# Optimization experiments

Measured on AMD Instinct MI355X. Metric: run time of the kernel, lower is better.

Reference implementation:

```python
import jax, jax.numpy as jnp
import numpy as np

N = 50000
E = 800000
D = 256
C = 8
H = 64
LN_EPS = 1e-5


def setup_inputs() -> dict:
    key = jax.random.key(0)
    ks = jax.random.split(key, 8)
    x = jax.random.normal(ks[0], (N, D), dtype=jnp.float32)
    edge_index = jax.random.randint(ks[1], (2, E), 0, N, dtype=jnp.int64)
    omega = jax.random.uniform(ks[2], (E, C), dtype=jnp.float32)
    # xavier-uniform-ish parameter init
    def xavier(k, shape, fan_in, fan_out):
        a = float(np.sqrt(6.0 / (fan_in + fan_out)))
        return jax.random.uniform(k, shape, dtype=jnp.float32, minval=-a, maxval=a)
    proj = xavier(ks[3], (D, C, H), D, C * H)          # layer-0 projection
    W1 = xavier(ks[4], (C, H, H), H, H)                # layer-0 channel weights
    W2 = xavier(ks[5], (C, H, H), H, H)                # layer-1 channel weights
    ln_gamma = jnp.ones((H,), dtype=jnp.float32)
    ln_beta = jnp.zeros((H,), dtype=jnp.float32)
    return {"x": x, "edge_index": edge_index, "omega": omega,
            "proj": proj, "W1": W1, "W2": W2,
            "ln_gamma": ln_gamma, "ln_beta": ln_beta}


def _conv(h, src, dst, omega, W):
    # h: [N, C, H]; per-channel weighted scatter-add then channel-specific bmm.
    outs = []
    for c in range(C):  # small fixed channel loop, mirrors original structure
        msg = omega[:, c, None] * h[src, c, :]                  # [E, H]
        outs.append(jax.ops.segment_sum(msg, dst, num_segments=N))
    h_next = jnp.stack(outs, axis=1)                            # [N, C, H]
    return jnp.einsum('nch,cho->nco', h_next, W)                # channel bmm


def _layernorm(h, gamma, beta):
    mu = jnp.mean(h, axis=-1, keepdims=True)
    var = jnp.mean(jnp.square(h - mu), axis=-1, keepdims=True)
    return (h - mu) * jax.lax.rsqrt(var + LN_EPS) * gamma + beta


def reference(x, edge_index, omega, proj, W1, W2, ln_gamma, ln_beta):
    src, dst = edge_index[0], edge_index[1]
    # layer 0: project raw features into channel space [N, C, H]
    h = (x @ proj.reshape(D, C * H)).reshape(N, C, H)
    h = _conv(h, src, dst, omega, W1)
    h = _layernorm(h, ln_gamma, ln_beta)
    h = jax.nn.relu(h)
    # layer 1 (last layer: no ReLU)
    h = _conv(h, src, dst, omega, W2)
    h = _layernorm(h, ln_gamma, ln_beta)
    return h
```

## Files before the change

### kernel.cpp

```cpp
#include <hip/hip_runtime.h>

#define NN 50000
#define NE 800000
#define DD 256
#define CC 8
#define HH 64
#define CHW 512
#define LN_EPS 1e-5f

typedef __attribute__((ext_vector_type(8))) __bf16 bf16x8;
typedef __attribute__((ext_vector_type(4))) float f32x4;

__device__ inline ushort f2bf(float f) {
  uint u = __float_as_uint(f);
  return (ushort)((u + 0x7fffu + ((u >> 16) & 1u)) >> 16);
}

__global__ __launch_bounds__(256) void fold_w1_kernel(
    const float* __restrict__ proj, const float* __restrict__ W1,
    ushort* __restrict__ projW1T) {
  __shared__ float wl[64];
  const int n = blockIdx.x;
  const int c = n >> 6, i = n & 63;
  const int tid = threadIdx.x;
  if (tid < 64) wl[tid] = W1[c * 4096 + tid * 64 + i];
  __syncthreads();
  const float* pr = proj + (size_t)tid * 512 + c * 64;
  float acc = 0.f;
#pragma unroll
  for (int k = 0; k < 64; ++k) acc += pr[k] * wl[k];
  projW1T[(size_t)n * 256 + tid] = f2bf(acc);
}

__global__ __launch_bounds__(256) void w2t_kernel(const float* __restrict__ W2,
                                                  ushort* __restrict__ W2T) {
  int c = blockIdx.x;
  for (int idx = threadIdx.x; idx < 4096; idx += 256) {
    int nn = idx >> 6, k = idx & 63;
    W2T[(size_t)c * 4096 + idx] = f2bf(W2[(size_t)c * 4096 + k * 64 + nn]);
  }
}

__global__ __launch_bounds__(256) void gemm_proj_kernel(
    const float* __restrict__ x, const ushort* __restrict__ BT,
    ushort* __restrict__ gout) {
  __shared__ ushort As[128 * 40];
  __shared__ ushort Bs[128 * 40];
  const int tid = threadIdx.x;
  const int lane = tid & 63, wv = tid >> 6;
  const int wm = wv >> 1, wn = wv & 1;
  const int lr = lane & 15, kg = lane >> 4;
  const int row0 = blockIdx.x * 128;
  const int col0 = blockIdx.y * 128;

  f32x4 acc[4][4];
#pragma unroll
  for (int i = 0; i < 4; ++i)
#pragma unroll
    for (int j = 0; j < 4; ++j) acc[i][j] = (f32x4){0.f, 0.f, 0.f, 0.f};

  for (int kk = 0; kk < 8; ++kk) {
    __syncthreads();
#pragma unroll
    for (int i = 0; i < 4; ++i) {
      int idx = tid + i * 256;
      int row = idx >> 3, quad = idx & 7;
      int rg = row0 + row;
      rg = rg < NN ? rg : NN - 1;
      float4 v = *(const float4*)(x + (size_t)rg * 256 + kk * 32 + quad * 4);
      ushort4 o = {f2bf(v.x), f2bf(v.y), f2bf(v.z), f2bf(v.w)};
      *(ushort4*)(As + row * 40 + quad * 4) = o;
    }
#pragma unroll
    for (int i = 0; i < 2; ++i) {
      int idx = tid + i * 256;
      int n = idx >> 2, quad = idx & 3;
      uint4 v = *(const uint4*)(BT + (size_t)(col0 + n) * 256 + kk * 32 + quad * 8);
      *(uint4*)(Bs + n * 40 + quad * 8) = v;
    }
    __syncthreads();
    bf16x8 a[4], b[4];
#pragma unroll
    for (int i = 0; i < 4; ++i)
      a[i] = *(const bf16x8*)(As + (wm * 64 + i * 16 + lr) * 40 + kg * 8);
#pragma unroll
    for (int j = 0; j < 4; ++j)
      b[j] = *(const bf16x8*)(Bs + (wn * 64 + j * 16 + lr) * 40 + kg * 8);
#pragma unroll
    for (int i = 0; i < 4; ++i)
#pragma unroll
      for (int j = 0; j < 4; ++j)
        acc[i][j] = __builtin_amdgcn_mfma_f32_16x16x32_bf16(a[i], b[j], acc[i][j], 0, 0, 0);
  }

  const int orow = kg * 4;
  const int ocol = lane & 15;
#pragma unroll
  for (int i = 0; i < 4; ++i) {
    int rg0 = row0 + wm * 64 + i * 16 + orow;
#pragma unroll
    for (int q = 0; q < 4; ++q) {
      int rg = rg0 + q;
      if (rg < NN) {
#pragma unroll
        for (int j = 0; j < 4; ++j) {
          gout[(size_t)rg * 512 + col0 + wn * 64 + j * 16 + ocol] = f2bf(acc[i][j][q]);
        }
      }
    }
  }
}

__global__ __launch_bounds__(256) void bmm_g_kernel(
    const ushort* __restrict__ h, const ushort* __restrict__ WT,
    ushort* __restrict__ g) {
  __shared__ ushort As[128 * 72];
  __shared__ ushort Bs[64 * 72];
  __shared__ float Cs[4][32 * 68];
  const int tid = threadIdx.x, lane = tid & 63, wv = tid >> 6;
  const int lr = lane & 15, kg = lane >> 4;
  const int n0 = blockIdx.x * 128;
  const int c = blockIdx.y;

#pragma unroll
  for (int i = 0; i < 4; ++i) {
    int idx = tid + i * 256;
    int row = idx >> 3, q = idx & 7;
    int rg = n0 + row;
    rg = rg < NN ? rg : NN - 1;
    *(uint4*)(As + row * 72 + q * 8) =
        *(const uint4*)(h + (size_t)rg * 512 + c * 64 + q * 8);
  }
#pragma unroll
  for (int i = 0; i < 2; ++i) {
    int idx = tid + i * 256;
    int row = idx >> 3, q = idx & 7;
    *(uint4*)(Bs + row * 72 + q * 8) =
        *(const uint4*)(WT + (size_t)c * 4096 + row * 64 + q * 8);
  }
  __syncthreads();

  f32x4 acc[2][4];
#pragma unroll
  for (int m = 0; m < 2; ++m)
#pragma unroll
    for (int j = 0; j < 4; ++j) acc[m][j] = (f32x4){0.f, 0.f, 0.f, 0.f};

#pragma unroll
  for (int ks = 0; ks < 2; ++ks) {
    bf16x8 a[2], b[4];
#pragma unroll
    for (int m = 0; m < 2; ++m)
      a[m] = *(const bf16x8*)(As + (wv * 32 + m * 16 + lr) * 72 + ks * 32 + kg * 8);
#pragma unroll
    for (int j = 0; j < 4; ++j)
      b[j] = *(const bf16x8*)(Bs + (j * 16 + lr) * 72 + ks * 32 + kg * 8);
#pragma unroll
    for (int m = 0; m < 2; ++m)
#pragma unroll
      for (int j = 0; j < 4; ++j)
        acc[m][j] = __builtin_amdgcn_mfma_f32_16x16x32_bf16(a[m], b[j], acc[m][j], 0, 0, 0);
  }

  float* cs = &Cs[wv][0];
#pragma unroll
  for (int m = 0; m < 2; ++m)
#pragma unroll
    for (int j = 0; j < 4; ++j)
#pragma unroll
      for (int q = 0; q < 4; ++q)
        cs[(m * 16 + kg * 4 + q) * 68 + j * 16 + lr] = acc[m][j][q];
  __syncthreads();

  const int row = lane & 31, half = lane >> 5;
  const int rg = n0 + wv * 32 + row;
  if (rg < NN) {
    const float* rp = cs + row * 68 + half * 32;
    ushort ob[32];
#pragma unroll
    for (int t = 0; t < 32; ++t) ob[t] = f2bf(rp[t]);
    ushort* op = g + (size_t)rg * 512 + c * 64 + half * 32;
#pragma unroll
    for (int t = 0; t < 4; ++t)
      *(uint4*)(op + t * 8) = *(uint4*)(ob + t * 8);
  }
}

__global__ void hist_kernel(const int* __restrict__ dst, int* __restrict__ cnt) {
  int e = blockIdx.x * 256 + threadIdx.x;
  if (e < NE) atomicAdd(&cnt[dst[e]], 1);
}

__global__ __launch_bounds__(1024) void scan_kernel(int* __restrict__ cntcur,
                                                    int* __restrict__ rowptr) {
  __shared__ int wsum[16];
  __shared__ int carry;
  int tid = threadIdx.x, lane = tid & 63, wv = tid >> 6;
  if (tid == 0) carry = 0;
  __syncthreads();
  for (int base = 0; base < NN; base += 1024) {
    int t = base + tid;
    int orig = (t < NN) ? cntcur[t] : 0;
    int v = orig;
#pragma unroll
    for (int off = 1; off < 64; off <<= 1) {
      int u = __shfl_up(v, off);
      if (lane >= off) v += u;
    }
    if (lane == 63) wsum[wv] = v;
    __syncthreads();
    if (tid < 16) {
      int s = wsum[tid];
#pragma unroll
      for (int off = 1; off < 16; off <<= 1) {
        int u = __shfl_up(s, off);
        if (tid >= off) s += u;
      }
      wsum[tid] = s;
    }
    __syncthreads();
    int run = carry;
    int excl = run + (wv ? wsum[wv - 1] : 0) + (v - orig);
    if (t < NN) {
      rowptr[t] = excl;
      cntcur[t] = excl;
    }
    int blocktotal = wsum[15];
    __syncthreads();
    if (tid == 0) carry = run + blocktotal;
    __syncthreads();
  }
  if (tid == 0) rowptr[NN] = carry;
}

__global__ void fill_kernel(const int* __restrict__ dst, const int* __restrict__ src,
                            const float* __restrict__ omega, int* __restrict__ cursor,
                            int* __restrict__ esrc, uint4* __restrict__ eom) {
  int e = blockIdx.x * 256 + threadIdx.x;
  if (e < NE) {
    int d = dst[e];
    int pos = atomicAdd(&cursor[d], 1);
    esrc[pos] = src[e];
    const float4* om4 = (const float4*)(omega + (size_t)e * 8);
    float4 o0 = om4[0], o1 = om4[1];
    union { _Float16 f[8]; uint4 v; } pk;
    pk.f[0] = (_Float16)o0.x; pk.f[1] = (_Float16)o0.y;
    pk.f[2] = (_Float16)o0.z; pk.f[3] = (_Float16)o0.w;
    pk.f[4] = (_Float16)o1.x; pk.f[5] = (_Float16)o1.y;
    pk.f[6] = (_Float16)o1.z; pk.f[7] = (_Float16)o1.w;
    eom[pos] = pk.v;
  }
}

template <bool RELU, bool BF16OUT>
__global__ __launch_bounds__(256) void conv_ln_kernel(
    const ushort* __restrict__ g, const int* __restrict__ esrc,
    const uint4* __restrict__ eom, const int* __restrict__ rowptr,
    const float* __restrict__ gamma, const float* __restrict__ beta,
    void* __restrict__ outv) {
  int n = blockIdx.x * 4 + (threadIdx.x >> 6);
  if (n >= NN) return;
  const int lane = threadIdx.x & 63;
  const int c = lane >> 3;
  const int i0 = (lane & 7) * 8;
  int start = rowptr[n], end = rowptr[n + 1];
  const uint4* g4 = (const uint4*)g;
  float acc[8] = {0.f, 0.f, 0.f, 0.f, 0.f, 0.f, 0.f, 0.f};
  for (int idx = start; idx < end; ++idx) {
    int s = esrc[idx];
    uint4 om = eom[idx];
    uint wd = (c & 2) ? ((c & 4) ? om.w : om.y) : ((c & 4) ? om.z : om.x);
    ushort hu = (c & 1) ? (ushort)(wd >> 16) : (ushort)(wd & 0xffffu);
    union { ushort u; _Float16 f; } cv; cv.u = hu;
    float w = (float)cv.f;
    uint4 hv = g4[(size_t)s * 64 + lane];
    acc[0] += w * __uint_as_float(hv.x << 16);
    acc[1] += w * __uint_as_float(hv.x & 0xffff0000u);
    acc[2] += w * __uint_as_float(hv.y << 16);
    acc[3] += w * __uint_as_float(hv.y & 0xffff0000u);
    acc[4] += w * __uint_as_float(hv.z << 16);
    acc[5] += w * __uint_as_float(hv.z & 0xffff0000u);
    acc[6] += w * __uint_as_float(hv.w << 16);
    acc[7] += w * __uint_as_float(hv.w & 0xffff0000u);
  }
  float s8 = ((acc[0] + acc[1]) + (acc[2] + acc[3])) +
             ((acc[4] + acc[5]) + (acc[6] + acc[7]));
  s8 += __shfl_xor(s8, 1);
  s8 += __shfl_xor(s8, 2);
  s8 += __shfl_xor(s8, 4);
  float mu = s8 * (1.f / 64.f);
  float d[8];
  float v = 0.f;
#pragma unroll
  for (int j = 0; j < 8; ++j) {
    d[j] = acc[j] - mu;
    v += d[j] * d[j];
  }
  v += __shfl_xor(v, 1);
  v += __shfl_xor(v, 2);
  v += __shfl_xor(v, 4);
  float inv = rsqrtf(v * (1.f / 64.f) + LN_EPS);
  float4 g0 = *(const float4*)(gamma + i0);
  float4 g1 = *(const float4*)(gamma + i0 + 4);
  float4 b0 = *(const float4*)(beta + i0);
  float4 b1 = *(const float4*)(beta + i0 + 4);
  float gg[8] = {g0.x, g0.y, g0.z, g0.w, g1.x, g1.y, g1.z, g1.w};
  float bb[8] = {b0.x, b0.y, b0.z, b0.w, b1.x, b1.y, b1.z, b1.w};
  float y[8];
#pragma unroll
  for (int j = 0; j < 8; ++j) {
    float t = d[j] * inv * gg[j] + bb[j];
    y[j] = RELU ? fmaxf(t, 0.f) : t;
  }
  if (BF16OUT) {
    ushort o[8];
#pragma unroll
    for (int j = 0; j < 8; ++j) o[j] = f2bf(y[j]);
    *(uint4*)((ushort*)outv + (size_t)n * 512 + c * 64 + i0) = *(uint4*)o;
  } else {
    float* op = (float*)outv + (size_t)n * 512 + c * 64 + i0;
    *(float4*)op = make_float4(y[0], y[1], y[2], y[3]);
    *(float4*)(op + 4) = make_float4(y[4], y[5], y[6], y[7]);
  }
}

extern "C" void kernel_launch(void* const* d_in, const int* in_sizes, int n_in,
                              void* d_out, int out_size, void* d_ws, size_t ws_size,
                              hipStream_t stream) {
  const float* x     = (const float*)d_in[0];
  const int*   edge  = (const int*)d_in[1];
  const float* omega = (const float*)d_in[2];
  const float* proj  = (const float*)d_in[3];
  const float* W1    = (const float*)d_in[4];
  const float* W2    = (const float*)d_in[5];
  const float* gamma = (const float*)d_in[6];
  const float* beta  = (const float*)d_in[7];
  const int* src = edge;
  const int* dst = edge + NE;

  char* p = (char*)d_ws;
  ushort* hbf    = (ushort*)p;              p += (size_t)NN * CHW * 2;
  uint4*  eom    = (uint4*)p;               p += (size_t)NE * 16;
  int*    esrc   = (int*)p;                 p += (size_t)NE * 4;
  int*    rowptr = (int*)p;                 p += (size_t)(NN + 16) * 4;
  int*    cntcur = (int*)p;                 p += (size_t)(NN + 16) * 4;
  ushort* projW1T= (ushort*)p;              p += (size_t)512 * 256 * 2;
  ushort* W2T    = (ushort*)p;

  ushort* h1 = (ushort*)d_out;

  hipMemsetAsync(cntcur, 0, NN * sizeof(int), stream);
  hist_kernel<<<(NE + 255) / 256, 256, 0, stream>>>(dst, cntcur);
  scan_kernel<<<1, 1024, 0, stream>>>(cntcur, rowptr);
  fill_kernel<<<(NE + 255) / 256, 256, 0, stream>>>(dst, src, omega, cntcur, esrc, eom);

  fold_w1_kernel<<<512, 256, 0, stream>>>(proj, W1, projW1T);
  w2t_kernel<<<8, 256, 0, stream>>>(W2, W2T);

  gemm_proj_kernel<<<dim3((NN + 127) / 128, 4), 256, 0, stream>>>(x, projW1T, hbf);
  conv_ln_kernel<true, true><<<(NN + 3) / 4, 256, 0, stream>>>(
      hbf, esrc, eom, rowptr, gamma, beta, h1);

  bmm_g_kernel<<<dim3((NN + 127) / 128, CC), 256, 0, stream>>>(h1, W2T, hbf);
  conv_ln_kernel<false, false><<<(NN + 3) / 4, 256, 0, stream>>>(
      hbf, esrc, eom, rowptr, gamma, beta, d_out);
}
```

Baseline: 503.1 us.

## Parallelize CSR prefix scan across blocks and unroll edge gather loop by four

Replaces the single-block serial scan over 50000 counts with a three-kernel reduce/scan/propagate scan spread over 49 blocks, which removes a long single-workgroup serial loop. The conv_ln edge loop is also unrolled by four so four neighbour-row gathers are in flight at once, hiding gather latency. The cost is two extra kernel launches, a small blocksum buffer, and higher register pressure in conv_ln.

Result: faster. 411.8 us (-18.2%).

```diff
diff --git a/kernel.cpp b/kernel.cpp
--- a/kernel.cpp
+++ b/kernel.cpp
@@ -7,6 +7,7 @@
 #define HH 64
 #define CHW 512
 #define LN_EPS 1e-5f
+#define SCAN_BLOCKS ((NN + 1023) / 1024)
 
 typedef __attribute__((ext_vector_type(8))) __bf16 bf16x8;
 typedef __attribute__((ext_vector_type(4))) float f32x4;
@@ -14,6 +15,24 @@
 __device__ inline ushort f2bf(float f) {
   uint u = __float_as_uint(f);
   return (ushort)((u + 0x7fffu + ((u >> 16) & 1u)) >> 16);
+}
+
+__device__ inline float om_decode(uint4 om, int c) {
+  uint wd = (c & 2) ? ((c & 4) ? om.w : om.y) : ((c & 4) ? om.z : om.x);
+  ushort hu = (c & 1) ? (ushort)(wd >> 16) : (ushort)(wd & 0xffffu);
+  union { ushort u; _Float16 f; } cv; cv.u = hu;
+  return (float)cv.f;
+}
+
+__device__ inline void acc8(float* acc, uint4 hv, float wt) {
+  acc[0] += wt * __uint_as_float(hv.x << 16);
+  acc[1] += wt * __uint_as_float(hv.x & 0xffff0000u);
+  acc[2] += wt * __uint_as_float(hv.y << 16);
+  acc[3] += wt * __uint_as_float(hv.y & 0xffff0000u);
+  acc[4] += wt * __uint_as_float(hv.z << 16);
+  acc[5] += wt * __uint_as_float(hv.z & 0xffff0000u);
+  acc[6] += wt * __uint_as_float(hv.w << 16);
+  acc[7] += wt * __uint_as_float(hv.w & 0xffff0000u);
 }
 
 __global__ __launch_bounds__(256) void fold_w1_kernel(
@@ -191,46 +210,67 @@
   if (e < NE) atomicAdd(&cnt[dst[e]], 1);
 }
 
-__global__ __launch_bounds__(1024) void scan_kernel(int* __restrict__ cntcur,
-                                                    int* __restrict__ rowptr) {
-  __shared__ int wsum[16];
-  __shared__ int carry;
+__global__ __launch_bounds__(1024) void scan1_kernel(const int* __restrict__ cnt,
+                                                     int* __restrict__ blocksum) {
+  __shared__ int ws[16];
+  int tid = threadIdx.x, t = blockIdx.x * 1024 + tid;
+  int v = (t < NN) ? cnt[t] : 0;
+#pragma unroll
+  for (int off = 32; off; off >>= 1) v += __shfl_xor(v, off);
+  if ((tid & 63) == 0) ws[tid >> 6] = v;
+  __syncthreads();
+  if (tid < 16) {
+    int s = ws[tid];
+#pragma unroll
+    for (int off = 8; off; off >>= 1) s += __shfl_xor(s, off, 16);
+    if (tid == 0) blocksum[blockIdx.x] = s;
+  }
+}
+
+__global__ __launch_bounds__(64) void scan2_kernel(int* __restrict__ blocksum,
+                                                   int* __restrict__ rowptr) {
+  int tid = threadIdx.x;
+  int v = (tid < SCAN_BLOCKS) ? blocksum[tid] : 0;
+  int orig = v;
+#pragma unroll
+  for (int off = 1; off < 64; off <<= 1) {
+    int u = __shfl_up(v, off);
+    if (tid >= off) v += u;
+  }
+  if (tid < SCAN_BLOCKS) blocksum[tid] = v - orig;
+  if (tid == 63) rowptr[NN] = v;
+}
+
+__global__ __launch_bounds__(1024) void scan3_kernel(const int* __restrict__ blocksum,
+                                                     int* __restrict__ cntcur,
+                                                     int* __restrict__ rowptr) {
+  __shared__ int ws[16];
   int tid = threadIdx.x, lane = tid & 63, wv = tid >> 6;
-  if (tid == 0) carry = 0;
-  __syncthreads();
-  for (int base = 0; base < NN; base += 1024) {
-    int t = base + tid;
-    int orig = (t < NN) ? cntcur[t] : 0;
-    int v = orig;
-#pragma unroll
-    for (int off = 1; off < 64; off <<= 1) {
-      int u = __shfl_up(v, off);
-      if (lane >= off) v += u;
+  int t = blockIdx.x * 1024 + tid;
+  int orig = (t < NN) ? cntcur[t] : 0;
+  int v = orig;
+#pragma unroll
+  for (int off = 1; off < 64; off <<= 1) {
+    int u = __shfl_up(v, off);
+    if (lane >= off) v += u;
+  }
+  if (lane == 63) ws[wv] = v;
+  __syncthreads();
+  if (tid < 16) {
+    int s = ws[tid];
+#pragma unroll
+    for (int off = 1; off < 16; off <<= 1) {
+      int u = __shfl_up(s, off, 16);
+      if (tid >= off) s += u;
     }
-    if (lane == 63) wsum[wv] = v;
-    __syncthreads();
-    if (tid < 16) {
-      int s = wsum[tid];
-#pragma unroll
-      for (int off = 1; off < 16; off <<= 1) {
-        int u = __shfl_up(s, off);
-        if (tid >= off) s += u;
-      }
-      wsum[tid] = s;
-    }
-    __syncthreads();
-    int run = carry;
-    int excl = run + (wv ? wsum[wv - 1] : 0) + (v - orig);
-    if (t < NN) {
-      rowptr[t] = excl;
-      cntcur[t] = excl;
-    }
-    int blocktotal = wsum[15];
-    __syncthreads();
-    if (tid == 0) carry = run + blocktotal;
-    __syncthreads();
-  }
-  if (tid == 0) rowptr[NN] = carry;
+    ws[tid] = s;
+  }
+  __syncthreads();
+  if (t < NN) {
+    int excl = blocksum[blockIdx.x] + (wv ? ws[wv - 1] : 0) + (v - orig);
+    rowptr[t] = excl;
+    cntcur[t] = excl;
+  }
 }
 
 __global__ void fill_kernel(const int* __restrict__ dst, const int* __restrict__ src,
@@ -266,23 +306,29 @@
   int start = rowptr[n], end = rowptr[n + 1];
   const uint4* g4 = (const uint4*)g;
   float acc[8] = {0.f, 0.f, 0.f, 0.f, 0.f, 0.f, 0.f, 0.f};
-  for (int idx = start; idx < end; ++idx) {
+
+  int idx = start;
+  for (; idx + 3 < end; idx += 4) {
+    int s0 = esrc[idx], s1 = esrc[idx + 1], s2 = esrc[idx + 2], s3 = esrc[idx + 3];
+    uint4 om0 = eom[idx], om1 = eom[idx + 1], om2 = eom[idx + 2], om3 = eom[idx + 3];
+    uint4 h0 = g4[(size_t)s0 * 64 + lane];
+    uint4 h1 = g4[(size_t)s1 * 64 + lane];
+    uint4 h2 = g4[(size_t)s2 * 64 + lane];
+    uint4 h3 = g4[(size_t)s3 * 64 + lane];
+    float w0 = om_decode(om0, c), w1 = om_decode(om1, c);
+    float w2 = om_decode(om2, c), w3 = om_decode(om3, c);
+    acc8(acc, h0, w0);
+    acc8(acc, h1, w1);
+    acc8(acc, h2, w2);
+    acc8(acc, h3, w3);
+  }
+  for (; idx < end; ++idx) {
     int s = esrc[idx];
     uint4 om = eom[idx];
-    uint wd = (c & 2) ? ((c & 4) ? om.w : om.y) : ((c & 4) ? om.z : om.x);
-    ushort hu = (c & 1) ? (ushort)(wd >> 16) : (ushort)(wd & 0xffffu);
-    union { ushort u; _Float16 f; } cv; cv.u = hu;
-    float w = (float)cv.f;
     uint4 hv = g4[(size_t)s * 64 + lane];
-    acc[0] += w * __uint_as_float(hv.x << 16);
-    acc[1] += w * __uint_as_float(hv.x & 0xffff0000u);
-    acc[2] += w * __uint_as_float(hv.y << 16);
-    acc[3] += w * __uint_as_float(hv.y & 0xffff0000u);
-    acc[4] += w * __uint_as_float(hv.z << 16);
-    acc[5] += w * __uint_as_float(hv.z & 0xffff0000u);
-    acc[6] += w * __uint_as_float(hv.w << 16);
-    acc[7] += w * __uint_as_float(hv.w & 0xffff0000u);
-  }
+    acc8(acc, hv, om_decode(om, c));
+  }
+
   float s8 = ((acc[0] + acc[1]) + (acc[2] + acc[3])) +
              ((acc[4] + acc[5]) + (acc[6] + acc[7]));
   s8 += __shfl_xor(s8, 1);
@@ -344,6 +390,7 @@
   int*    esrc   = (int*)p;                 p += (size_t)NE * 4;
   int*    rowptr = (int*)p;                 p += (size_t)(NN + 16) * 4;
   int*    cntcur = (int*)p;                 p += (size_t)(NN + 16) * 4;
+  int*    blocksum=(int*)p;                 p += (size_t)64 * 4;
   ushort* projW1T= (ushort*)p;              p += (size_t)512 * 256 * 2;
   ushort* W2T    = (ushort*)p;
 
@@ -351,7 +398,9 @@
 
   hipMemsetAsync(cntcur, 0, NN * sizeof(int), stream);
   hist_kernel<<<(NE + 255) / 256, 256, 0, stream>>>(dst, cntcur);
-  scan_kernel<<<1, 1024, 0, stream>>>(cntcur, rowptr);
+  scan1_kernel<<<SCAN_BLOCKS, 1024, 0, stream>>>(cntcur, blocksum);
+  scan2_kernel<<<1, 64, 0, stream>>>(blocksum, rowptr);
+  scan3_kernel<<<SCAN_BLOCKS, 1024, 0, stream>>>(blocksum, cntcur, rowptr);
   fill_kernel<<<(NE + 255) / 256, 256, 0, stream>>>(dst, src, omega, cntcur, esrc, eom);
 
   fold_w1_kernel<<<512, 256, 0, stream>>>(proj, W1, projW1T);
```
